# Optimization experiments

Measured on AMD Instinct MI355X. Metric: run time of the kernel, lower is better.

Reference implementation:

```python
import jax, jax.numpy as jnp
import numpy as np

C_IN = 64
H = 32          # h_channels
HEADS = 8
HC = H * HEADS  # 256
C_OUT = 64
EPS = 1e-5


def conv1x1(w, x):
    # 1x1 Conv1d == per-position GEMM: w [O, C], x [B, C, L] -> [B, O, L]
    return jnp.einsum('oc,bcl->bol', w, x)


def batchnorm1d(x, gamma, beta):
    # training-mode BatchNorm1d: stats over (batch, length), biased variance
    mean = jnp.mean(x, axis=(0, 2), keepdims=True)
    var = jnp.mean(jnp.square(x - mean), axis=(0, 2), keepdims=True)
    xhat = (x - mean) * jax.lax.rsqrt(var + EPS)
    return xhat * gamma[None, :, None] + beta[None, :, None]


def setup_inputs() -> dict:
    key = jax.random.key(0)
    ks = jax.random.split(key, 6)
    B, L = 16, 8192
    s_in = 1.0 / np.sqrt(C_IN)
    s_hc = 1.0 / np.sqrt(HC)
    return {
        'x':  jax.random.normal(ks[0], (B, C_IN, L), dtype=jnp.float32),
        'wk': jax.random.uniform(ks[1], (HC, C_IN), jnp.float32, -s_in, s_in),
        'wq': jax.random.uniform(ks[2], (HC, C_IN), jnp.float32, -s_in, s_in),
        'wv': jax.random.uniform(ks[3], (HC, C_IN), jnp.float32, -s_in, s_in),
        'wc': jax.random.uniform(ks[4], (C_IN, HC), jnp.float32, -s_hc, s_hc),
        'g1': jnp.ones((C_IN,), jnp.float32),
        'b1': jnp.zeros((C_IN,), jnp.float32),
        'wl': jax.random.uniform(ks[5], (C_OUT, C_IN), jnp.float32, -s_in, s_in),
        'g2': jnp.ones((C_OUT,), jnp.float32),
        'b2': jnp.zeros((C_OUT,), jnp.float32),
    }


def reference(x, wk, wq, wv, wc, g1, b1, wl, g2, b2):
    k = conv1x1(wk, x)  # [B, HC, L]
    q = conv1x1(wq, x)
    v = conv1x1(wv, x)
    # channel-wise attention: q @ k^T over length -> [B, HC, HC]
    scores = jnp.einsum('bil,bjl->bij', q, k)
    attn = jax.nn.softmax(scores, axis=1)  # softmax over dim=1 (rows), as in source
    att_vec = jnp.einsum('bij,bjl->bil', attn, v) / np.sqrt(H).astype(np.float32)
    out = conv1x1(wc, att_vec)            # [B, C_IN, L]
    out = batchnorm1d(out, g1, b1) + x    # residual
    out = batchnorm1d(conv1x1(wl, out), g2, b2)
    return jax.nn.relu(out)
```

## Files before the change

### kernel.cpp

```cpp
#include <hip/hip_runtime.h>
#include <math.h>

#define TB 16
#define TL 8192
#define TC 64

constexpr float INV_BL = 1.0f / (16.0f * 8192.0f);
constexpr float EPSV = 1e-5f;
constexpr float INV_SQRT_H = 0.17677669529663687f;

#define WS_G      0
#define WS_SX     65536
#define WS_STATS  66560
#define WS_M      66816
#define WS_N      132352
#define WS_S1T    197888
#define WS_V1P    460032
#define WS_GPART  4654336
#define WS_SXPART 8848640
#define WS_MPART  8914176
#define WS_WKT    9962752

typedef __attribute__((ext_vector_type(8))) short short8v;
typedef __attribute__((ext_vector_type(4))) float f32x4;

__device__ __forceinline__ ushort bf16rne(float f){
  uint u = __float_as_uint(f);
  u += 0x7FFF + ((u >> 16) & 1);
  return (ushort)(u >> 16);
}

__device__ __forceinline__ int fraddr(int ch, int g){
  return ch*128 + 8*(g ^ (ch & 7));
}

__global__ __launch_bounds__(256) void k1_gram(const float* __restrict__ x,
                                               float* __restrict__ ws){
  __shared__ ushort Xh[64*128];
  __shared__ ushort Xl[64*128];
  const int b = blockIdx.y, chunk = blockIdx.x;
  const int t = threadIdx.x;
  const int lane = t & 63;
  const int w = __builtin_amdgcn_readfirstlane(t >> 6);
  const float* xb = x + (size_t)b*TC*TL + (size_t)chunk*128;
  const int ch = t >> 2, q = t & 3;
  float sx = 0.f;
  float4 rgv[8];
  #pragma unroll
  for (int gg=0; gg<4; ++gg){
    rgv[2*gg]   = *(const float4*)(xb + ch*TL + q*32 + 8*gg);
    rgv[2*gg+1] = *(const float4*)(xb + ch*TL + q*32 + 8*gg + 4);
  }
  #pragma unroll
  for (int gg=0; gg<4; ++gg){
    const float4 v0 = rgv[2*gg], v1 = rgv[2*gg+1];
    const float ff[8] = {v0.x,v0.y,v0.z,v0.w,v1.x,v1.y,v1.z,v1.w};
    union { short8v v; ushort u[8]; } hh, ll;
    #pragma unroll
    for (int i=0;i<8;++i){
      sx += ff[i];
      const ushort hv = bf16rne(ff[i]);
      hh.u[i] = hv;
      ll.u[i] = bf16rne(ff[i] - __uint_as_float(((uint)hv)<<16));
    }
    const int g = q*4 + gg;
    const int wa = ch*128 + 8*(g ^ (ch & 7));
    *(short8v*)&Xh[wa] = hh.v;
    *(short8v*)&Xl[wa] = ll.v;
  }
  __syncthreads();
  const int rA = w*16 + (lane & 15);
  const int gq = lane >> 4;
  f32x4 acc0={0.f,0.f,0.f,0.f}, acc1={0.f,0.f,0.f,0.f},
        acc2={0.f,0.f,0.f,0.f}, acc3={0.f,0.f,0.f,0.f};
  #pragma unroll
  for (int kk=0; kk<4; ++kk){
    const int g = kk*4 + gq;
    const short8v Ah = *(const short8v*)&Xh[fraddr(rA, g)];
    const short8v Al = *(const short8v*)&Xl[fraddr(rA, g)];
    const int rB = (lane & 15);
    const short8v Bh0 = *(const short8v*)&Xh[fraddr(rB,      g)];
    const short8v Bl0 = *(const short8v*)&Xl[fraddr(rB,      g)];
    const short8v Bh1 = *(const short8v*)&Xh[fraddr(rB + 16, g)];
    const short8v Bl1 = *(const short8v*)&Xl[fraddr(rB + 16, g)];
    const short8v Bh2 = *(const short8v*)&Xh[fraddr(rB + 32, g)];
    const short8v Bl2 = *(const short8v*)&Xl[fraddr(rB + 32, g)];
    const short8v Bh3 = *(const short8v*)&Xh[fraddr(rB + 48, g)];
    const short8v Bl3 = *(const short8v*)&Xl[fraddr(rB + 48, g)];
    acc0 = __builtin_amdgcn_mfma_f32_16x16x32_bf16(Ah, Bh0, acc0, 0, 0, 0);
    acc0 = __builtin_amdgcn_mfma_f32_16x16x32_bf16(Ah, Bl0, acc0, 0, 0, 0);
    acc0 = __builtin_amdgcn_mfma_f32_16x16x32_bf16(Al, Bh0, acc0, 0, 0, 0);
    acc0 = __builtin_amdgcn_mfma_f32_16x16x32_bf16(Al, Bl0, acc0, 0, 0, 0);
    acc1 = __builtin_amdgcn_mfma_f32_16x16x32_bf16(Ah, Bh1, acc1, 0, 0, 0);
    acc1 = __builtin_amdgcn_mfma_f32_16x16x32_bf16(Ah, Bl1, acc1, 0, 0, 0);
    acc1 = __builtin_amdgcn_mfma_f32_16x16x32_bf16(Al, Bh1, acc1, 0, 0, 0);
    acc1 = __builtin_amdgcn_mfma_f32_16x16x32_bf16(Al, Bl1, acc1, 0, 0, 0);
    acc2 = __builtin_amdgcn_mfma_f32_16x16x32_bf16(Ah, Bh2, acc2, 0, 0, 0);
    acc2 = __builtin_amdgcn_mfma_f32_16x16x32_bf16(Ah, Bl2, acc2, 0, 0, 0);
    acc2 = __builtin_amdgcn_mfma_f32_16x16x32_bf16(Al, Bh2, acc2, 0, 0, 0);
    acc2 = __builtin_amdgcn_mfma_f32_16x16x32_bf16(Al, Bl2, acc2, 0, 0, 0);
    acc3 = __builtin_amdgcn_mfma_f32_16x16x32_bf16(Ah, Bh3, acc3, 0, 0, 0);
    acc3 = __builtin_amdgcn_mfma_f32_16x16x32_bf16(Ah, Bl3, acc3, 0, 0, 0);
    acc3 = __builtin_amdgcn_mfma_f32_16x16x32_bf16(Al, Bh3, acc3, 0, 0, 0);
    acc3 = __builtin_amdgcn_mfma_f32_16x16x32_bf16(Al, Bl3, acc3, 0, 0, 0);
  }
  float* Gp = ws + WS_GPART + (size_t)(b*64 + chunk)*4096;
  const int col = lane & 15, rq = lane >> 4;
  #pragma unroll
  for (int r=0;r<4;++r){
    const int row = (w*16 + rq*4 + r)*64;
    Gp[row +  0 + col] = acc0[r];
    Gp[row + 16 + col] = acc1[r];
    Gp[row + 32 + col] = acc2[r];
    Gp[row + 48 + col] = acc3[r];
  }
  sx += __shfl_xor(sx, 1, 4);
  sx += __shfl_xor(sx, 2, 4);
  if (q == 0){
    ws[WS_SXPART + (b*64+chunk)*64 + ch] = sx;
  }
}

__global__ __launch_bounds__(256) void kA1(const float* __restrict__ wk,
                                           float* __restrict__ ws){
  const int p = blockIdx.x, b = blockIdx.y;
  const int t = threadIdx.x;
  const float* Gp = ws + WS_GPART + (size_t)b*64*4096 + p*256 + t;
  float s = 0.f;
  #pragma unroll 8
  for (int ch=0; ch<64; ++ch) s += Gp[(size_t)ch*4096];
  ws[WS_G + b*4096 + p*256 + t] = s;
  if (p==0 && t<64){
    float sv = 0.f;
    #pragma unroll 8
    for (int ch=0; ch<64; ++ch) sv += ws[WS_SXPART + (b*64+ch)*64 + t];
    ws[WS_SX + b*64 + t] = sv;
  }
  if (p==0 && b==0) ws[WS_STATS + t] = 0.f;
  if (b==0){
    const int j = 16*p + (t>>4), k0 = (t&15)*4;
    const float4 v = *(const float4*)(wk + j*64 + k0);
    ws[WS_WKT + (k0+0)*256 + j] = v.x;
    ws[WS_WKT + (k0+1)*256 + j] = v.y;
    ws[WS_WKT + (k0+2)*256 + j] = v.z;
    ws[WS_WKT + (k0+3)*256 + j] = v.w;
  }
}

__global__ __launch_bounds__(256) void kA2(const float* __restrict__ wq,
                                           float* __restrict__ ws){
  __shared__ float Gt[64*68];
  const int b = blockIdx.y, iblk = blockIdx.x;
  const int t = threadIdx.x;
  const float* G = ws + WS_G + b*4096;
  #pragma unroll
  for (int r=0;r<4;++r){
    const int idx = r*1024 + t*4;
    *(float4*)&Gt[(idx>>6)*68 + (idx&63)] = *(const float4*)(G + idx);
  }
  __syncthreads();
  const int il = t>>4, cq = t&15;
  const int i = iblk*16 + il;
  const float* wqr = wq + i*64;
  float4 a0={0,0,0,0};
  #pragma unroll 8
  for (int k=0;k<64;++k){
    const float a = wqr[k];
    const float4 g0 = *(const float4*)&Gt[k*68 + cq*4];
    a0.x=fmaf(a,g0.x,a0.x); a0.y=fmaf(a,g0.y,a0.y); a0.z=fmaf(a,g0.z,a0.z); a0.w=fmaf(a,g0.w,a0.w);
  }
  float* S1T = ws + WS_S1T + b*16384;
  S1T[(cq*4+0)*256 + i]=a0.x;
  S1T[(cq*4+1)*256 + i]=a0.y;
  S1T[(cq*4+2)*256 + i]=a0.z;
  S1T[(cq*4+3)*256 + i]=a0.w;
}

__global__ __launch_bounds__(256) void kb12(const float* __restrict__ wv,
                                            float* __restrict__ ws){
  __shared__ float scl[256*17];
  __shared__ float pstat[256];
  __shared__ float fstat[32];
  const int b = blockIdx.y, jp = blockIdx.x;
  const int j0 = jp*16;
  const int t = threadIdx.x;
  const float* S1Tb = ws + WS_S1T + b*16384;
  const float* wkT = ws + WS_WKT;
  float sc[16];
  #pragma unroll
  for (int jj=0;jj<16;++jj) sc[jj]=0.f;
  #pragma unroll 4
  for (int k=0;k<64;++k){
    const float s1 = S1Tb[k*256 + t];
    const float4 w0 = *(const float4*)(wkT + k*256 + j0);
    const float4 w1 = *(const float4*)(wkT + k*256 + j0 + 4);
    const float4 w2 = *(const float4*)(wkT + k*256 + j0 + 8);
    const float4 w3 = *(const float4*)(wkT + k*256 + j0 + 12);
    sc[ 0]=fmaf(w0.x,s1,sc[ 0]); sc[ 1]=fmaf(w0.y,s1,sc[ 1]); sc[ 2]=fmaf(w0.z,s1,sc[ 2]); sc[ 3]=fmaf(w0.w,s1,sc[ 3]);
    sc[ 4]=fmaf(w1.x,s1,sc[ 4]); sc[ 5]=fmaf(w1.y,s1,sc[ 5]); sc[ 6]=fmaf(w1.z,s1,sc[ 6]); sc[ 7]=fmaf(w1.w,s1,sc[ 7]);
    sc[ 8]=fmaf(w2.x,s1,sc[ 8]); sc[ 9]=fmaf(w2.y,s1,sc[ 9]); sc[10]=fmaf(w2.z,s1,sc[10]); sc[11]=fmaf(w2.w,s1,sc[11]);
    sc[12]=fmaf(w3.x,s1,sc[12]); sc[13]=fmaf(w3.y,s1,sc[13]); sc[14]=fmaf(w3.z,s1,sc[14]); sc[15]=fmaf(w3.w,s1,sc[15]);
  }
  #pragma unroll
  for (int jj=0;jj<16;++jj) scl[t*17+jj] = sc[jj];
  __syncthreads();
  const int col = t&15, ig = t>>4;
  {
    float m = -3.0e38f;
    #pragma unroll
    for (int q=0;q<16;++q) m = fmaxf(m, scl[(ig*16+q)*17 + col]);
    pstat[ig*16+col] = m;
  }
  __syncthreads();
  if (t<16){
    float m = -3.0e38f;
    #pragma unroll
    for (int q=0;q<16;++q) m = fmaxf(m, pstat[q*16+t]);
    fstat[t] = m;
  }
  __syncthreads();
  {
    const float mj = fstat[col];
    float s = 0.f;
    #pragma unroll
    for (int q=0;q<16;++q) s += __expf(scl[(ig*16+q)*17 + col] - mj);
    pstat[ig*16+col] = s;
  }
  __syncthreads();
  if (t<16){
    float s = 0.f;
    #pragma unroll
    for (int q=0;q<16;++q) s += pstat[q*16+t];
    fstat[16+t] = 1.f/s;
  }
  __syncthreads();
  #pragma unroll
  for (int jj=0;jj<16;++jj)
    sc[jj] = __expf(sc[jj] - fstat[jj]) * fstat[16+jj];
  float* Vp = ws + WS_V1P + (size_t)(b*16 + jp)*16384 + t*64;
  #pragma unroll
  for (int cb=0; cb<4; ++cb){
    float acc[16];
    #pragma unroll
    for (int cc=0;cc<16;++cc) acc[cc]=0.f;
    #pragma unroll
    for (int jj=0;jj<16;++jj){
      const float p = sc[jj];
      const float* wvr = wv + (j0+jj)*64 + cb*16;
      #pragma unroll
      for (int cc=0;cc<16;++cc)
        acc[cc] = fmaf(p, wvr[cc], acc[cc]);
    }
    #pragma unroll
    for (int g=0; g<4; ++g){
      float4 v; v.x=acc[4*g]; v.y=acc[4*g+1]; v.z=acc[4*g+2]; v.w=acc[4*g+3];
      *(float4*)&Vp[cb*16 + 4*g] = v;
    }
  }
}

__global__ __launch_bounds__(256) void kc_mpart(const float* __restrict__ wc,
                                                float* __restrict__ ws){
  __shared__ float V1l[16*65];
  const int b = blockIdx.y, kq = blockIdx.x;
  const int t = threadIdx.x;
  #pragma unroll
  for (int r=0;r<4;++r){
    const int e = t + 256*r;
    const int c = e & 63, il = e >> 6;
    const float* Vp = ws + WS_V1P + (size_t)b*16*16384 + (kq*16+il)*64 + c;
    float s = 0.f;
    #pragma unroll
    for (int jp=0;jp<16;++jp) s += Vp[jp*16384];
    V1l[il*65 + c] = s * INV_SQRT_H;
  }
  __syncthreads();
  const int c = t & 63;
  const int og = __builtin_amdgcn_readfirstlane(t >> 6);
  float acc[16];
  #pragma unroll
  for (int oo=0;oo<16;++oo) acc[oo]=0.f;
  #pragma unroll
  for (int il=0; il<16; ++il){
    const float v = V1l[il*65 + c];
    const float* wcr = wc + (og*16)*256 + kq*16 + il;
    #pragma unroll
    for (int oo=0;oo<16;++oo)
      acc[oo] = fmaf(wcr[oo*256], v, acc[oo]);
  }
  float* Mp = ws + WS_MPART + (size_t)(b*16 + kq)*4096;
  #pragma unroll
  for (int oo=0;oo<16;++oo)
    Mp[(og*16+oo)*64 + c] = acc[oo];
}

__global__ __launch_bounds__(256) void kd_stats1(float* __restrict__ ws){
  __shared__ float Msub[4*65];
  __shared__ float Gl[64*67];
  __shared__ float Sxl[64];
  const int b = blockIdx.y, oq = blockIdx.x;
  const int t = threadIdx.x;
  const int o = t >> 6, lane = t & 63;
  const int row = oq*4 + o;
  {
    const float* Mp = ws + WS_MPART + (size_t)b*16*4096 + row*64 + lane;
    float s = 0.f;
    #pragma unroll
    for (int kq=0;kq<16;++kq) s += Mp[kq*4096];
    ws[WS_M + b*4096 + row*64 + lane] = s;
    Msub[o*65 + lane] = s;
  }
  #pragma unroll
  for (int r=0;r<16;++r){
    const int e = t + 256*r;
    Gl[(e>>6)*67 + (e&63)] = ws[WS_G + b*4096 + e];
  }
  if (t<64) Sxl[t] = ws[WS_SX + b*64 + t];
  __syncthreads();
  float sk = 0.f;
  #pragma unroll 4
  for (int c=0;c<64;++c) sk = fmaf(Gl[lane*67+c], Msub[o*65+c], sk);
  float d = Msub[o*65 + lane] * sk;
  float s1 = Msub[o*65 + lane] * Sxl[lane];
  #pragma unroll
  for (int off=1; off<64; off<<=1){
    d  += __shfl_xor(d,  off);
    s1 += __shfl_xor(s1, off);
  }
  if (lane==0){
    atomicAdd(&ws[WS_STATS + row], s1);
    atomicAdd(&ws[WS_STATS + 64 + row], d);
  }
}

__global__ __launch_bounds__(256) void ke_n_stats2(const float* __restrict__ wl,
                                                   const float* __restrict__ g1,
                                                   float* __restrict__ ws){
  __shared__ float Ml[64*65];
  __shared__ float Gl[64*67];
  __shared__ float Nsub[4*65];
  __shared__ float Sxl[64], a1l[64];
  const int b = blockIdx.y, oq = blockIdx.x;
  const int t = threadIdx.x;
  const int o = t >> 6, lane = t & 63;
  const int row = oq*4 + o;
  if (t<64){
    const float mean1 = ws[WS_STATS+t]*INV_BL;
    const float var1 = ws[WS_STATS+64+t]*INV_BL - mean1*mean1;
    a1l[t] = g1[t]*rsqrtf(var1 + EPSV);
    Sxl[t] = ws[WS_SX + b*64 + t];
  }
  #pragma unroll
  for (int r=0;r<16;++r){
    const int e = t + 256*r;
    Ml[(e>>6)*65 + (e&63)] = ws[WS_M + b*4096 + e];
    Gl[(e>>6)*67 + (e&63)] = ws[WS_G + b*4096 + e];
  }
  __syncthreads();
  float acc = 0.f;
  #pragma unroll 4
  for (int k=0;k<64;++k){
    const float wk_ = wl[row*64 + k] * a1l[k];
    acc = fmaf(wk_, Ml[k*65 + lane], acc);
  }
  const float nv = acc + wl[row*64 + lane];
  ws[WS_N + b*4096 + row*64 + lane] = nv;
  Nsub[o*65 + lane] = nv;
  __syncthreads();
  float sk = 0.f;
  #pragma unroll 4
  for (int c=0;c<64;++c) sk = fmaf(Gl[lane*67+c], Nsub[o*65+c], sk);
  float d = Nsub[o*65 + lane] * sk;
  float s2 = Nsub[o*65 + lane] * Sxl[lane];
  #pragma unroll
  for (int off=1; off<64; off<<=1){
    d  += __shfl_xor(d,  off);
    s2 += __shfl_xor(s2, off);
  }
  if (lane==0){
    atomicAdd(&ws[WS_STATS + 128 + row], s2);
    atomicAdd(&ws[WS_STATS + 192 + row], d);
  }
}

__global__ __launch_bounds__(512) void k3_out(const float* __restrict__ x,
                                              const float* __restrict__ g2,
                                              const float* __restrict__ b2,
                                              const float* __restrict__ ws,
                                              float* __restrict__ out){
  __shared__ ushort Xh[128*72];
  __shared__ ushort Xl[128*72];
  __shared__ ushort Nh[64*72];
  __shared__ ushort Nl2[64*72];
  __shared__ float a2l[64], el[64];
  const int b = blockIdx.y, lc = blockIdx.x;
  const int t = threadIdx.x;
  const int chs = t>>3, qs = t&7;
  const float* xw = x + (size_t)b*TC*TL + lc*128;
  float4 rgv[4];
  #pragma unroll
  for (int i=0;i<4;++i)
    rgv[i] = *(const float4*)(xw + (size_t)chs*TL + qs*16 + 4*i);
  if (t<64){
    const float mu = ws[WS_STATS+128+t]*INV_BL;
    const float var2 = ws[WS_STATS+192+t]*INV_BL - mu*mu;
    const float a2 = g2[t]*rsqrtf(var2 + EPSV);
    a2l[t] = a2;
    el[t] = b2[t] - a2*mu;
  }
  {
    const float* Nsrc = ws + WS_N + b*4096;
    #pragma unroll
    for (int r=0;r<8;++r){
      const int e = t + 512*r;
      const int o = e>>6, c = e&63;
      const float nv = Nsrc[e];
      const ushort h = bf16rne(nv);
      Nh[o*72 + c] = h;
      Nl2[o*72 + c] = bf16rne(nv - __uint_as_float(((uint)h)<<16));
    }
  }
  #pragma unroll
  for (int i=0;i<4;++i){
    const float fv[4] = {rgv[i].x, rgv[i].y, rgv[i].z, rgv[i].w};
    #pragma unroll
    for (int j=0;j<4;++j){
      const int l = qs*16 + 4*i + j;
      const int pos = 8*((chs>>3) ^ ((l>>4)&7)) + (chs&7);
      const ushort h = bf16rne(fv[j]);
      Xh[l*72 + pos] = h;
      Xl[l*72 + pos] = bf16rne(fv[j] - __uint_as_float(((uint)h)<<16));
    }
  }
  __syncthreads();
  const int w = __builtin_amdgcn_readfirstlane(t >> 6);
  const int lane = t & 63;
  const int orow = lane & 15, gq = lane >> 4;
  const int lrow = w*16 + orow;
  f32x4 acc[4];
  #pragma unroll
  for (int i=0;i<4;++i){ acc[i][0]=0.f; acc[i][1]=0.f; acc[i][2]=0.f; acc[i][3]=0.f; }
  #pragma unroll
  for (int ks=0; ks<2; ++ks){
    const int g = ks*4 + gq;
    const int xoff = lrow*72 + 8*(g ^ w);
    const short8v bh = *(const short8v*)&Xh[xoff];
    const short8v bl = *(const short8v*)&Xl[xoff];
    const int cb = g*8;
    #pragma unroll
    for (int ot=0; ot<4; ++ot){
      const short8v ah = *(const short8v*)&Nh[(ot*16+orow)*72 + cb];
      const short8v al = *(const short8v*)&Nl2[(ot*16+orow)*72 + cb];
      acc[ot] = __builtin_amdgcn_mfma_f32_16x16x32_bf16(ah, bh, acc[ot], 0, 0, 0);
      acc[ot] = __builtin_amdgcn_mfma_f32_16x16x32_bf16(ah, bl, acc[ot], 0, 0, 0);
      acc[ot] = __builtin_amdgcn_mfma_f32_16x16x32_bf16(al, bh, acc[ot], 0, 0, 0);
      acc[ot] = __builtin_amdgcn_mfma_f32_16x16x32_bf16(al, bl, acc[ot], 0, 0, 0);
    }
  }
  const int l = lc*128 + w*16 + orow;
  #pragma unroll
  for (int ot=0; ot<4; ++ot){
    #pragma unroll
    for (int r=0;r<4;++r){
      const int o = ot*16 + gq*4 + r;
      const float v = fmaxf(fmaf(a2l[o], acc[ot][r], el[o]), 0.f);
      out[(size_t)(b*TC + o)*TL + l] = v;
    }
  }
}

extern "C" void kernel_launch(void* const* d_in, const int* in_sizes, int n_in,
                              void* d_out, int out_size, void* d_ws, size_t ws_size,
                              hipStream_t stream){
  const float* x  = (const float*)d_in[0];
  const float* wk = (const float*)d_in[1];
  const float* wq = (const float*)d_in[2];
  const float* wv = (const float*)d_in[3];
  const float* wc = (const float*)d_in[4];
  const float* g1 = (const float*)d_in[5];
  const float* wl = (const float*)d_in[7];
  const float* g2 = (const float*)d_in[8];
  const float* b2 = (const float*)d_in[9];
  float* out = (float*)d_out;
  float* ws  = (float*)d_ws;

  k1_gram    <<<dim3(64,16), 256, 0, stream>>>(x, ws);
  kA1        <<<dim3(16,16), 256, 0, stream>>>(wk, ws);
  kA2        <<<dim3(16,16), 256, 0, stream>>>(wq, ws);
  kb12       <<<dim3(16,16), 256, 0, stream>>>(wv, ws);
  kc_mpart   <<<dim3(16,16), 256, 0, stream>>>(wc, ws);
  kd_stats1  <<<dim3(16,16), 256, 0, stream>>>(ws);
  ke_n_stats2<<<dim3(16,16), 256, 0, stream>>>(wl, g1, ws);
  k3_out     <<<dim3(64,16), 512, 0, stream>>>(x, g2, b2, ws, out);
}
```

Before: 91.84 us.

## Process two L-chunks per block in gram and output kernels with prefetch

```diff
diff --git a/kernel.cpp b/kernel.cpp
--- a/kernel.cpp
+++ b/kernel.cpp
@@ -17,9 +17,9 @@
 #define WS_S1T    197888
 #define WS_V1P    460032
 #define WS_GPART  4654336
-#define WS_SXPART 8848640
-#define WS_MPART  8914176
-#define WS_WKT    9962752
+#define WS_SXPART 6751488
+#define WS_MPART  6784256
+#define WS_WKT    7832832
 
 typedef __attribute__((ext_vector_type(8))) short short8v;
 typedef __attribute__((ext_vector_type(4))) float f32x4;
@@ -42,9 +42,14 @@
   const int t = threadIdx.x;
   const int lane = t & 63;
   const int w = __builtin_amdgcn_readfirstlane(t >> 6);
-  const float* xb = x + (size_t)b*TC*TL + (size_t)chunk*128;
+  const float* xb = x + (size_t)b*TC*TL + (size_t)chunk*256;
   const int ch = t >> 2, q = t & 3;
   float sx = 0.f;
+  const int rA = w*16 + (lane & 15);
+  const int rB = lane & 15;
+  const int gq = lane >> 4;
+  f32x4 acc0={0.f,0.f,0.f,0.f}, acc1={0.f,0.f,0.f,0.f},
+        acc2={0.f,0.f,0.f,0.f}, acc3={0.f,0.f,0.f,0.f};
   float4 rgv[8];
   #pragma unroll
   for (int gg=0; gg<4; ++gg){
@@ -69,16 +74,17 @@
     *(short8v*)&Xl[wa] = ll.v;
   }
   __syncthreads();
-  const int rA = w*16 + (lane & 15);
-  const int gq = lane >> 4;
-  f32x4 acc0={0.f,0.f,0.f,0.f}, acc1={0.f,0.f,0.f,0.f},
-        acc2={0.f,0.f,0.f,0.f}, acc3={0.f,0.f,0.f,0.f};
+  float4 rg2[8];
+  #pragma unroll
+  for (int gg=0; gg<4; ++gg){
+    rg2[2*gg]   = *(const float4*)(xb + ch*TL + 128 + q*32 + 8*gg);
+    rg2[2*gg+1] = *(const float4*)(xb + ch*TL + 128 + q*32 + 8*gg + 4);
+  }
   #pragma unroll
   for (int kk=0; kk<4; ++kk){
     const int g = kk*4 + gq;
     const short8v Ah = *(const short8v*)&Xh[fraddr(rA, g)];
     const short8v Al = *(const short8v*)&Xl[fraddr(rA, g)];
-    const int rB = (lane & 15);
     const short8v Bh0 = *(const short8v*)&Xh[fraddr(rB,      g)];
     const short8v Bl0 = *(const short8v*)&Xl[fraddr(rB,      g)];
     const short8v Bh1 = *(const short8v*)&Xh[fraddr(rB + 16, g)];
@@ -104,7 +110,56 @@
     acc3 = __builtin_amdgcn_mfma_f32_16x16x32_bf16(Al, Bh3, acc3, 0, 0, 0);
     acc3 = __builtin_amdgcn_mfma_f32_16x16x32_bf16(Al, Bl3, acc3, 0, 0, 0);
   }
-  float* Gp = ws + WS_GPART + (size_t)(b*64 + chunk)*4096;
+  __syncthreads();
+  #pragma unroll
+  for (int gg=0; gg<4; ++gg){
+    const float4 v0 = rg2[2*gg], v1 = rg2[2*gg+1];
+    const float ff[8] = {v0.x,v0.y,v0.z,v0.w,v1.x,v1.y,v1.z,v1.w};
+    union { short8v v; ushort u[8]; } hh, ll;
+    #pragma unroll
+    for (int i=0;i<8;++i){
+      sx += ff[i];
+      const ushort hv = bf16rne(ff[i]);
+      hh.u[i] = hv;
+      ll.u[i] = bf16rne(ff[i] - __uint_as_float(((uint)hv)<<16));
+    }
+    const int g = q*4 + gg;
+    const int wa = ch*128 + 8*(g ^ (ch & 7));
+    *(short8v*)&Xh[wa] = hh.v;
+    *(short8v*)&Xl[wa] = ll.v;
+  }
+  __syncthreads();
+  #pragma unroll
+  for (int kk=0; kk<4; ++kk){
+    const int g = kk*4 + gq;
+    const short8v Ah = *(const short8v*)&Xh[fraddr(rA, g)];
+    const short8v Al = *(const short8v*)&Xl[fraddr(rA, g)];
+    const short8v Bh0 = *(const short8v*)&Xh[fraddr(rB,      g)];
+    const short8v Bl0 = *(const short8v*)&Xl[fraddr(rB,      g)];
+    const short8v Bh1 = *(const short8v*)&Xh[fraddr(rB + 16, g)];
+    const short8v Bl1 = *(const short8v*)&Xl[fraddr(rB + 16, g)];
+    const short8v Bh2 = *(const short8v*)&Xh[fraddr(rB + 32, g)];
+    const short8v Bl2 = *(const short8v*)&Xl[fraddr(rB + 32, g)];
+    const short8v Bh3 = *(const short8v*)&Xh[fraddr(rB + 48, g)];
+    const short8v Bl3 = *(const short8v*)&Xl[fraddr(rB + 48, g)];
+    acc0 = __builtin_amdgcn_mfma_f32_16x16x32_bf16(Ah, Bh0, acc0, 0, 0, 0);
+    acc0 = __builtin_amdgcn_mfma_f32_16x16x32_bf16(Ah, Bl0, acc0, 0, 0, 0);
+    acc0 = __builtin_amdgcn_mfma_f32_16x16x32_bf16(Al, Bh0, acc0, 0, 0, 0);
+    acc0 = __builtin_amdgcn_mfma_f32_16x16x32_bf16(Al, Bl0, acc0, 0, 0, 0);
+    acc1 = __builtin_amdgcn_mfma_f32_16x16x32_bf16(Ah, Bh1, acc1, 0, 0, 0);
+    acc1 = __builtin_amdgcn_mfma_f32_16x16x32_bf16(Ah, Bl1, acc1, 0, 0, 0);
+    acc1 = __builtin_amdgcn_mfma_f32_16x16x32_bf16(Al, Bh1, acc1, 0, 0, 0);
+    acc1 = __builtin_amdgcn_mfma_f32_16x16x32_bf16(Al, Bl1, acc1, 0, 0, 0);
+    acc2 = __builtin_amdgcn_mfma_f32_16x16x32_bf16(Ah, Bh2, acc2, 0, 0, 0);
+    acc2 = __builtin_amdgcn_mfma_f32_16x16x32_bf16(Ah, Bl2, acc2, 0, 0, 0);
+    acc2 = __builtin_amdgcn_mfma_f32_16x16x32_bf16(Al, Bh2, acc2, 0, 0, 0);
+    acc2 = __builtin_amdgcn_mfma_f32_16x16x32_bf16(Al, Bl2, acc2, 0, 0, 0);
+    acc3 = __builtin_amdgcn_mfma_f32_16x16x32_bf16(Ah, Bh3, acc3, 0, 0, 0);
+    acc3 = __builtin_amdgcn_mfma_f32_16x16x32_bf16(Ah, Bl3, acc3, 0, 0, 0);
+    acc3 = __builtin_amdgcn_mfma_f32_16x16x32_bf16(Al, Bh3, acc3, 0, 0, 0);
+    acc3 = __builtin_amdgcn_mfma_f32_16x16x32_bf16(Al, Bl3, acc3, 0, 0, 0);
+  }
+  float* Gp = ws + WS_GPART + (size_t)(b*32 + chunk)*4096;
   const int col = lane & 15, rq = lane >> 4;
   #pragma unroll
   for (int r=0;r<4;++r){
@@ -117,7 +172,7 @@
   sx += __shfl_xor(sx, 1, 4);
   sx += __shfl_xor(sx, 2, 4);
   if (q == 0){
-    ws[WS_SXPART + (b*64+chunk)*64 + ch] = sx;
+    ws[WS_SXPART + (b*32+chunk)*64 + ch] = sx;
   }
 }
 
@@ -125,15 +180,15 @@
                                            float* __restrict__ ws){
   const int p = blockIdx.x, b = blockIdx.y;
   const int t = threadIdx.x;
-  const float* Gp = ws + WS_GPART + (size_t)b*64*4096 + p*256 + t;
+  const float* Gp = ws + WS_GPART + (size_t)b*32*4096 + p*256 + t;
   float s = 0.f;
   #pragma unroll 8
-  for (int ch=0; ch<64; ++ch) s += Gp[(size_t)ch*4096];
+  for (int ch=0; ch<32; ++ch) s += Gp[(size_t)ch*4096];
   ws[WS_G + b*4096 + p*256 + t] = s;
   if (p==0 && t<64){
     float sv = 0.f;
     #pragma unroll 8
-    for (int ch=0; ch<64; ++ch) sv += ws[WS_SXPART + (b*64+ch)*64 + t];
+    for (int ch=0; ch<32; ++ch) sv += ws[WS_SXPART + (b*32+ch)*64 + t];
     ws[WS_SX + b*64 + t] = sv;
   }
   if (p==0 && b==0) ws[WS_STATS + t] = 0.f;
@@ -393,10 +448,10 @@
   __shared__ ushort Nh[64*72];
   __shared__ ushort Nl2[64*72];
   __shared__ float a2l[64], el[64];
-  const int b = blockIdx.y, lc = blockIdx.x;
+  const int b = blockIdx.y, lc2 = blockIdx.x;
   const int t = threadIdx.x;
   const int chs = t>>3, qs = t&7;
-  const float* xw = x + (size_t)b*TC*TL + lc*128;
+  const float* xw = x + (size_t)b*TC*TL + (size_t)lc2*256;
   float4 rgv[4];
   #pragma unroll
   for (int i=0;i<4;++i)
@@ -420,52 +475,60 @@
       Nl2[o*72 + c] = bf16rne(nv - __uint_as_float(((uint)h)<<16));
     }
   }
-  #pragma unroll
-  for (int i=0;i<4;++i){
-    const float fv[4] = {rgv[i].x, rgv[i].y, rgv[i].z, rgv[i].w};
-    #pragma unroll
-    for (int j=0;j<4;++j){
-      const int l = qs*16 + 4*i + j;
-      const int pos = 8*((chs>>3) ^ ((l>>4)&7)) + (chs&7);
-      const ushort h = bf16rne(fv[j]);
-      Xh[l*72 + pos] = h;
-      Xl[l*72 + pos] = bf16rne(fv[j] - __uint_as_float(((uint)h)<<16));
-    }
-  }
-  __syncthreads();
   const int w = __builtin_amdgcn_readfirstlane(t >> 6);
   const int lane = t & 63;
   const int orow = lane & 15, gq = lane >> 4;
   const int lrow = w*16 + orow;
-  f32x4 acc[4];
-  #pragma unroll
-  for (int i=0;i<4;++i){ acc[i][0]=0.f; acc[i][1]=0.f; acc[i][2]=0.f; acc[i][3]=0.f; }
-  #pragma unroll
-  for (int ks=0; ks<2; ++ks){
-    const int g = ks*4 + gq;
-    const int xoff = lrow*72 + 8*(g ^ w);
-    const short8v bh = *(const short8v*)&Xh[xoff];
-    const short8v bl = *(const short8v*)&Xl[xoff];
-    const int cb = g*8;
+  for (int win=0; win<2; ++win){
+    #pragma unroll
+    for (int i=0;i<4;++i){
+      const float fv[4] = {rgv[i].x, rgv[i].y, rgv[i].z, rgv[i].w};
+      #pragma unroll
+      for (int j=0;j<4;++j){
+        const int l = qs*16 + 4*i + j;
+        const int pos = 8*((chs>>3) ^ ((l>>4)&7)) + (chs&7);
+        const ushort h = bf16rne(fv[j]);
+        Xh[l*72 + pos] = h;
+        Xl[l*72 + pos] = bf16rne(fv[j] - __uint_as_float(((uint)h)<<16));
+      }
+    }
+    __syncthreads();
+    if (win==0){
+      #pragma unroll
+      for (int i=0;i<4;++i)
+        rgv[i] = *(const float4*)(xw + 128 + (size_t)chs*TL + qs*16 + 4*i);
+    }
+    f32x4 acc[4];
+    #pragma unroll
+    for (int i=0;i<4;++i){ acc[i][0]=0.f; acc[i][1]=0.f; acc[i][2]=0.f; acc[i][3]=0.f; }
+    #pragma unroll
+    for (int ks=0; ks<2; ++ks){
+      const int g = ks*4 + gq;
+      const int xoff = lrow*72 + 8*(g ^ w);
+      const short8v bh = *(const short8v*)&Xh[xoff];
+      const short8v bl = *(const short8v*)&Xl[xoff];
+      const int cb = g*8;
+      #pragma unroll
+      for (int ot=0; ot<4; ++ot){
+        const short8v ah = *(const short8v*)&Nh[(ot*16+orow)*72 + cb];
+        const short8v al = *(const short8v*)&Nl2[(ot*16+orow)*72 + cb];
+        acc[ot] = __builtin_amdgcn_mfma_f32_16x16x32_bf16(ah, bh, acc[ot], 0, 0, 0);
+        acc[ot] = __builtin_amdgcn_mfma_f32_16x16x32_bf16(ah, bl, acc[ot], 0, 0, 0);
+        acc[ot] = __builtin_amdgcn_mfma_f32_16x16x32_bf16(al, bh, acc[ot], 0, 0, 0);
+        acc[ot] = __builtin_amdgcn_mfma_f32_16x16x32_bf16(al, bl, acc[ot], 0, 0, 0);
+      }
+    }
+    const int l = lc2*256 + win*128 + w*16 + orow;
     #pragma unroll
     for (int ot=0; ot<4; ++ot){
-      const short8v ah = *(const short8v*)&Nh[(ot*16+orow)*72 + cb];
-      const short8v al = *(const short8v*)&Nl2[(ot*16+orow)*72 + cb];
-      acc[ot] = __builtin_amdgcn_mfma_f32_16x16x32_bf16(ah, bh, acc[ot], 0, 0, 0);
-      acc[ot] = __builtin_amdgcn_mfma_f32_16x16x32_bf16(ah, bl, acc[ot], 0, 0, 0);
-      acc[ot] = __builtin_amdgcn_mfma_f32_16x16x32_bf16(al, bh, acc[ot], 0, 0, 0);
-      acc[ot] = __builtin_amdgcn_mfma_f32_16x16x32_bf16(al, bl, acc[ot], 0, 0, 0);
-    }
-  }
-  const int l = lc*128 + w*16 + orow;
-  #pragma unroll
-  for (int ot=0; ot<4; ++ot){
-    #pragma unroll
-    for (int r=0;r<4;++r){
-      const int o = ot*16 + gq*4 + r;
-      const float v = fmaxf(fmaf(a2l[o], acc[ot][r], el[o]), 0.f);
-      out[(size_t)(b*TC + o)*TL + l] = v;
-    }
+      #pragma unroll
+      for (int r=0;r<4;++r){
+        const int o = ot*16 + gq*4 + r;
+        const float v = fmaxf(fmaf(a2l[o], acc[ot][r], el[o]), 0.f);
+        out[(size_t)(b*TC + o)*TL + l] = v;
+      }
+    }
+    if (win==0) __syncthreads();
   }
 }
 
@@ -484,12 +547,12 @@
   float* out = (float*)d_out;
   float* ws  = (float*)d_ws;
 
-  k1_gram    <<<dim3(64,16), 256, 0, stream>>>(x, ws);
+  k1_gram    <<<dim3(32,16), 256, 0, stream>>>(x, ws);
   kA1        <<<dim3(16,16), 256, 0, stream>>>(wk, ws);
   kA2        <<<dim3(16,16), 256, 0, stream>>>(wq, ws);
   kb12       <<<dim3(16,16), 256, 0, stream>>>(wv, ws);
   kc_mpart   <<<dim3(16,16), 256, 0, stream>>>(wc, ws);
   kd_stats1  <<<dim3(16,16), 256, 0, stream>>>(ws);
   ke_n_stats2<<<dim3(16,16), 256, 0, stream>>>(wl, g1, ws);
-  k3_out     <<<dim3(64,16), 512, 0, stream>>>(x, g2, b2, ws, out);
-}
+  k3_out     <<<dim3(32,16), 512, 0, stream>>>(x, g2, b2, ws, out);
+}
```

Measured after the change: 86.57 us (median of 2 runs). 5.7% less time.
